# Optimization experiments

Hardware: AMD Instinct MI355X
Metric: run time of the kernel (lower is better)

The kernel has to match this reference:

```python
import jax, jax.numpy as jnp
import numpy as np

N_NODES = 50000
IN_CH = 256
Z_DIM = 64
N_EDGES = 800000


def setup_inputs() -> dict:
    key = jax.random.key(0)
    k_x, k_e, k_wm, k_ws = jax.random.split(key, 4)
    x = jax.random.normal(k_x, (N_NODES, IN_CH), dtype=jnp.float32)
    edge_index = jax.random.randint(k_e, (2, N_EDGES), 0, N_NODES, dtype=jnp.int64)
    # Glorot-style init like PyG GCNConv
    scale = 1.0 / np.sqrt(IN_CH)
    W_mu = jax.random.uniform(k_wm, (IN_CH, Z_DIM), dtype=jnp.float32, minval=-scale, maxval=scale)
    W_logstd = jax.random.uniform(k_ws, (IN_CH, Z_DIM), dtype=jnp.float32, minval=-scale, maxval=scale)
    b_mu = jnp.zeros((Z_DIM,), dtype=jnp.float32)
    b_logstd = jnp.zeros((Z_DIM,), dtype=jnp.float32)
    return {"x": x, "edge_index": edge_index, "W_mu": W_mu, "b_mu": b_mu,
            "W_logstd": W_logstd, "b_logstd": b_logstd}


def _gcn_conv(x, W, b, src, dst, deg_inv_sqrt, num_nodes):
    # PyG GCNConv: out = D^{-1/2} (A + I) D^{-1/2} X W + b
    xw = x @ W                                   # [N, Z]
    norm = deg_inv_sqrt[src] * deg_inv_sqrt[dst]  # [E+N]
    msg = xw[src] * norm[:, None]                 # gather + scale, [E+N, Z]
    agg = jax.ops.segment_sum(msg, dst, num_segments=num_nodes)  # scatter-add
    return agg + b


def reference(x, edge_index, W_mu, b_mu, W_logstd, b_logstd):
    num_nodes = x.shape[0]
    loops = jnp.arange(num_nodes, dtype=edge_index.dtype)
    src = jnp.concatenate([edge_index[0], loops])
    dst = jnp.concatenate([edge_index[1], loops])
    # degree (with self loops) on target nodes, symmetric normalization
    deg = jax.ops.segment_sum(jnp.ones_like(dst, dtype=x.dtype), dst, num_segments=num_nodes)
    deg_inv_sqrt = jnp.where(deg > 0, jax.lax.rsqrt(jnp.maximum(deg, 1.0)), 0.0)
    mu = _gcn_conv(x, W_mu, b_mu, src, dst, deg_inv_sqrt, num_nodes)
    logstd = _gcn_conv(x, W_logstd, b_logstd, src, dst, deg_inv_sqrt, num_nodes)
    return (mu, logstd)
```

## Files before the change

kernel.cpp:

```cpp
#include <hip/hip_runtime.h>

#define N_NODES 50000
#define IN_CH   256
#define Z_DIM   64
#define N_EDGES 800000
#define CH2     128
#define NODE_OFF (N_NODES * Z_DIM)
#define SEG     8
#define SEGN    50048
#define NBUCKET (SEG * SEGN)
#define CAP     16
#define CAPN    64
#define ECHUNKS (N_EDGES / 256)
#define TM      128
#define GTILES  ((N_NODES + TM - 1) / TM)
#define DBLK    ((N_NODES + 31) / 32)
#define NW      32768

typedef __bf16 bf16x8 __attribute__((ext_vector_type(8)));
typedef float  f32x4  __attribute__((ext_vector_type(4)));

__device__ __forceinline__ unsigned short f2bf(float f) {
    __bf16 h = (__bf16)f;
    unsigned short u;
    __builtin_memcpy(&u, &h, 2);
    return u;
}
__device__ __forceinline__ float bf_lo(unsigned w) { return __uint_as_float(w << 16); }
__device__ __forceinline__ float bf_hi(unsigned w) { return __uint_as_float(w & 0xFFFF0000u); }

__global__ void k_pre(int* __restrict__ cur8,
                      const float* __restrict__ Wmu, const float* __restrict__ Wls,
                      unsigned short* __restrict__ WbT) {
    int g = blockIdx.x * 256 + threadIdx.x;
    if (g < NBUCKET) cur8[g] = 0;
    int h = g - NBUCKET;
    if (h >= 0 && h < NW) {
        int n = h >> 8, k = h & 255;
        float v = (n < 64) ? Wmu[(size_t)k * 64 + n] : Wls[(size_t)k * 64 + (n - 64)];
        WbT[(size_t)n * 256 + k] = f2bf(v);
    }
}

#define CSP2 136
__device__ __forceinline__ void gemm_tile(int t, const float* __restrict__ x,
                                          const unsigned short* __restrict__ WbT,
                                          unsigned short* __restrict__ xwb,
                                          unsigned short* As) {
    const int tid = threadIdx.x;
    const int r0  = t * TM;

    {
        int row_l0 = tid >> 3;
        int cb     = (tid & 7) * 32;
#pragma unroll
        for (int r = 0; r < 4; ++r) {
            int row_l = r * 32 + row_l0;
            int row   = r0 + row_l;
            char* dpb = (char*)As + row_l * 512;
            unsigned cswz = (unsigned)((row_l & 7) << 4);
            if (row < N_NODES) {
                const float4* xp = (const float4*)(x + (size_t)row * IN_CH + cb);
#pragma unroll
                for (int i = 0; i < 4; ++i) {
                    float4 a = xp[2 * i];
                    float4 b = xp[2 * i + 1];
                    uint4 w;
                    w.x = (unsigned)f2bf(a.x) | ((unsigned)f2bf(a.y) << 16);
                    w.y = (unsigned)f2bf(a.z) | ((unsigned)f2bf(a.w) << 16);
                    w.z = (unsigned)f2bf(b.x) | ((unsigned)f2bf(b.y) << 16);
                    w.w = (unsigned)f2bf(b.z) | ((unsigned)f2bf(b.w) << 16);
                    *(uint4*)(dpb + (((unsigned)(cb * 2 + i * 16)) ^ cswz)) = w;
                }
            } else {
                uint4 z = make_uint4(0, 0, 0, 0);
#pragma unroll
                for (int i = 0; i < 4; ++i)
                    *(uint4*)(dpb + (((unsigned)(cb * 2 + i * 16)) ^ cswz)) = z;
            }
        }
    }
    __syncthreads();

    const int wv    = tid >> 6;
    const int lane  = tid & 63;
    const int m     = lane & 15;
    const int q     = lane >> 4;
    const int rbase = wv * 32;

    f32x4 acc[2][8] = {};
    const char* apb0 = (const char*)As + (rbase + m) * 512;
    const char* apb1 = apb0 + 16 * 512;
    const unsigned   sw  = (unsigned)((m & 7) << 4);
    const unsigned short* bp = WbT + (size_t)m * 256 + q * 8;

#pragma unroll
    for (int k0 = 0; k0 < IN_CH; k0 += 32) {
        unsigned off = ((unsigned)(q * 16 + 2 * k0)) ^ sw;
        bf16x8 a0 = *(const bf16x8*)(apb0 + off);
        bf16x8 a1 = *(const bf16x8*)(apb1 + off);
#pragma unroll
        for (int nt = 0; nt < 8; ++nt) {
            bf16x8 bf_ = *(const bf16x8*)(bp + (size_t)nt * 16 * 256 + k0);
            acc[0][nt] = __builtin_amdgcn_mfma_f32_16x16x32_bf16(a0, bf_, acc[0][nt], 0, 0, 0);
            acc[1][nt] = __builtin_amdgcn_mfma_f32_16x16x32_bf16(a1, bf_, acc[1][nt], 0, 0, 0);
        }
    }

    __syncthreads();
    {
        unsigned short* Css = As;
#pragma unroll
        for (int mi = 0; mi < 2; ++mi)
#pragma unroll
            for (int nt = 0; nt < 8; ++nt)
#pragma unroll
                for (int r = 0; r < 4; ++r)
                    Css[(rbase + mi * 16 + q * 4 + r) * CSP2 + nt * 16 + m] =
                        f2bf(acc[mi][nt][r]);
    }
    __syncthreads();
    {
        int row_l = tid >> 2;
        int c0    = (tid & 3) * 32;
#pragma unroll
        for (int rr = 0; rr < 2; ++rr) {
            int rl  = rr * 64 + row_l;
            int row = r0 + rl;
            if (row < N_NODES) {
                const uint4* cp = (const uint4*)(As + rl * CSP2 + c0);
                uint4 w0 = cp[0];
                uint4 w1 = cp[1];
                uint4 w2 = cp[2];
                uint4 w3 = cp[3];
                uint4* op = (uint4*)(xwb + (size_t)row * CH2 + c0);
                op[0] = w0; op[1] = w1; op[2] = w2; op[3] = w3;
            }
        }
    }
}

__global__ __launch_bounds__(256, 2) void k_gemm_scat(
    const float* __restrict__ x, const unsigned short* __restrict__ WbT,
    unsigned short* __restrict__ xwb,
    const int* __restrict__ src, const int* __restrict__ dst,
    int* __restrict__ cur8, unsigned short* __restrict__ pk2) {
    __shared__ __align__(16) unsigned short As[TM * 256];
    if (blockIdx.x < GTILES) {
        gemm_tile(blockIdx.x, x, WbT, xwb, As);
    } else {
        int c = blockIdx.x - GTILES;
        int e = c * 256 + threadIdx.x;
        int s = src[e];
        int d = dst[e];
        int idx = (c & (SEG - 1)) * SEGN + d;
        int pos = atomicAdd(&cur8[idx], 1);
        if (pos < CAP) pk2[(size_t)idx * CAP + pos] = (unsigned short)s;
    }
}

__global__ __launch_bounds__(256) void k_dinv(const int* __restrict__ cur8,
                                              const unsigned short* __restrict__ pk2,
                                              float* __restrict__ dinv,
                                              unsigned short* __restrict__ plist,
                                              unsigned short* __restrict__ degc) {
    const int i = blockIdx.x * 32 + (threadIdx.x >> 3);
    const int s = threadIdx.x & 7;
    if (i >= N_NODES) return;

    int cnt = cur8[s * SEGN + i];
    int cc  = (cnt > CAP) ? CAP : cnt;

    int run = cc;
#pragma unroll
    for (int k = 1; k < 8; k <<= 1) {
        int v = __shfl_up(run, k, 8);
        if (s >= k) run += v;
    }
    int tot = cnt;
#pragma unroll
    for (int k = 1; k < 8; k <<= 1) tot += __shfl_xor(tot, k, 8);

    int total_c = __shfl(run, 7, 8);

    int off = run - cc;
    int lim = CAPN - off;
    if (lim < 0) lim = 0;
    if (cc > lim) cc = lim;

    const unsigned short* sp = pk2 + ((size_t)(s * SEGN + i)) * CAP;
    unsigned short*       dp = plist + (size_t)i * CAPN + off;
    for (int j = 0; j < cc; ++j) dp[j] = sp[j];

    if (s == 0) {
        dinv[i] = rsqrtf((float)(1 + tot));
        degc[i] = (unsigned short)((total_c > CAPN) ? CAPN : total_c);
    }
}

__global__ __launch_bounds__(256) void k_gather(const unsigned short* __restrict__ plist,
                                                const unsigned short* __restrict__ degc,
                                                const unsigned short* __restrict__ xwb,
                                                const float* __restrict__ dinv,
                                                const float* __restrict__ bmu,
                                                const float* __restrict__ bls,
                                                float* __restrict__ out) {
    const int i  = blockIdx.x * 16 + (threadIdx.x >> 4);
    const int cl = threadIdx.x & 15;

    const float di  = dinv[i];
    const int   deg = degc[i];

    float acc[8];
    {
        float sq = di * di;
        uint4 w = *(const uint4*)(xwb + (size_t)i * CH2 + cl * 8);
        acc[0] = bf_lo(w.x) * sq; acc[1] = bf_hi(w.x) * sq;
        acc[2] = bf_lo(w.y) * sq; acc[3] = bf_hi(w.y) * sq;
        acc[4] = bf_lo(w.z) * sq; acc[5] = bf_hi(w.z) * sq;
        acc[6] = bf_lo(w.w) * sq; acc[7] = bf_hi(w.w) * sq;
    }

    const unsigned short* lp = plist + (size_t)i * CAPN;
    for (int j = 0; j < deg; j += 4) {
        uint2 pe = *(const uint2*)(lp + j);
        int s0 = (int)(pe.x & 0xFFFFu);
        int s1 = (int)(pe.x >> 16);
        int s2 = (int)(pe.y & 0xFFFFu);
        int s3 = (int)(pe.y >> 16);
        int rem = deg - j;
        int e1 = (rem > 1) ? s1 : s0;
        int e2 = (rem > 2) ? s2 : s0;
        int e3 = (rem > 3) ? s3 : s0;
        float n0 = di * dinv[s0];
        float n1 = (rem > 1) ? di * dinv[e1] : 0.f;
        float n2 = (rem > 2) ? di * dinv[e2] : 0.f;
        float n3 = (rem > 3) ? di * dinv[e3] : 0.f;
        const uint4 w0 = *(const uint4*)(xwb + (size_t)s0 * CH2 + cl * 8);
        const uint4 w1 = *(const uint4*)(xwb + (size_t)e1 * CH2 + cl * 8);
        const uint4 w2 = *(const uint4*)(xwb + (size_t)e2 * CH2 + cl * 8);
        const uint4 w3 = *(const uint4*)(xwb + (size_t)e3 * CH2 + cl * 8);
        acc[0] += bf_lo(w0.x) * n0 + bf_lo(w1.x) * n1 + bf_lo(w2.x) * n2 + bf_lo(w3.x) * n3;
        acc[1] += bf_hi(w0.x) * n0 + bf_hi(w1.x) * n1 + bf_hi(w2.x) * n2 + bf_hi(w3.x) * n3;
        acc[2] += bf_lo(w0.y) * n0 + bf_lo(w1.y) * n1 + bf_lo(w2.y) * n2 + bf_lo(w3.y) * n3;
        acc[3] += bf_hi(w0.y) * n0 + bf_hi(w1.y) * n1 + bf_hi(w2.y) * n2 + bf_hi(w3.y) * n3;
        acc[4] += bf_lo(w0.z) * n0 + bf_lo(w1.z) * n1 + bf_lo(w2.z) * n2 + bf_lo(w3.z) * n3;
        acc[5] += bf_hi(w0.z) * n0 + bf_hi(w1.z) * n1 + bf_hi(w2.z) * n2 + bf_hi(w3.z) * n3;
        acc[6] += bf_lo(w0.w) * n0 + bf_lo(w1.w) * n1 + bf_lo(w2.w) * n2 + bf_lo(w3.w) * n3;
        acc[7] += bf_hi(w0.w) * n0 + bf_hi(w1.w) * n1 + bf_hi(w2.w) * n2 + bf_hi(w3.w) * n3;
    }

    {
        int c0 = cl * 8;
        const float* bb = (c0 < 64) ? (bmu + c0) : (bls + (c0 - 64));
        float4 b0 = *(const float4*)(bb + 0);
        float4 b1 = *(const float4*)(bb + 4);
        float* o = (c0 < 64) ? (out + (size_t)i * 64 + c0)
                             : (out + NODE_OFF + (size_t)i * 64 + (c0 - 64));
        *(float4*)(o + 0) = make_float4(acc[0] + b0.x, acc[1] + b0.y,
                                        acc[2] + b0.z, acc[3] + b0.w);
        *(float4*)(o + 4) = make_float4(acc[4] + b1.x, acc[5] + b1.y,
                                        acc[6] + b1.z, acc[7] + b1.w);
    }
}

extern "C" void kernel_launch(void* const* d_in, const int* in_sizes, int n_in,
                              void* d_out, int out_size, void* d_ws, size_t ws_size,
                              hipStream_t stream) {
    const float* x   = (const float*)d_in[0];
    const int*   ei  = (const int*)d_in[1];
    const float* Wmu = (const float*)d_in[2];
    const float* bmu = (const float*)d_in[3];
    const float* Wls = (const float*)d_in[4];
    const float* bls = (const float*)d_in[5];
    float* out = (float*)d_out;

    const int* src = ei;
    const int* dst = ei + N_EDGES;

    char* ws = (char*)d_ws;
    int*            cur8  = (int*)(ws + 0);
    float*          dinv  = (float*)(ws + 1638400);
    unsigned short* WbT   = (unsigned short*)(ws + 1867776);
    unsigned short* pk2   = (unsigned short*)(ws + 2097152);
    unsigned short* xwb   = (unsigned short*)(ws + 16777216);
    unsigned short* plist = (unsigned short*)(ws + 29577216);
    unsigned short* degc  = (unsigned short*)(ws + 35977216);

    k_pre<<<(NBUCKET + NW + 255) / 256, 256, 0, stream>>>(cur8, Wmu, Wls, WbT);
    k_gemm_scat<<<GTILES + ECHUNKS, 256, 0, stream>>>(x, WbT, xwb, src, dst, cur8, pk2);
    k_dinv<<<DBLK, 256, 0, stream>>>(cur8, pk2, dinv, plist, degc);
    k_gather<<<N_NODES / 16, 256, 0, stream>>>(plist, degc, xwb, dinv, bmu, bls, out);
}
```

Baseline: 183.5 us.

## Fuse degree/list build and gather into one persistent kernel with grid barrier

Merges the k_dinv and k_gather kernels into a single persistent kernel with a fixed grid of 1792 blocks that grid-strides over nodes, joined by a software grid-wide barrier built on agent-scope atomics. The barrier counters are reset in k_pre. This removes one kernel launch and the drain and refill between the two phases, in exchange for spin-wait overhead, reliance on all 1792 blocks being co-resident (a bounded spin is the only guard against deadlock), and lower parallelism from the fixed grid.

```diff
diff --git a/kernel.cpp b/kernel.cpp
--- a/kernel.cpp
+++ b/kernel.cpp
@@ -14,8 +14,8 @@
 #define ECHUNKS (N_EDGES / 256)
 #define TM      128
 #define GTILES  ((N_NODES + TM - 1) / TM)
-#define DBLK    ((N_NODES + 31) / 32)
 #define NW      32768
+#define GRID_B  1792
 
 typedef __bf16 bf16x8 __attribute__((ext_vector_type(8)));
 typedef float  f32x4  __attribute__((ext_vector_type(4)));
@@ -31,9 +31,10 @@
 
 __global__ void k_pre(int* __restrict__ cur8,
                       const float* __restrict__ Wmu, const float* __restrict__ Wls,
-                      unsigned short* __restrict__ WbT) {
+                      unsigned short* __restrict__ WbT, int* __restrict__ bar) {
     int g = blockIdx.x * 256 + threadIdx.x;
     if (g < NBUCKET) cur8[g] = 0;
+    if (g < 2) bar[g] = 0;
     int h = g - NBUCKET;
     if (h >= 0 && h < NW) {
         int n = h >> 8, k = h & 255;
@@ -159,108 +160,129 @@
     }
 }
 
-__global__ __launch_bounds__(256) void k_dinv(const int* __restrict__ cur8,
-                                              const unsigned short* __restrict__ pk2,
-                                              float* __restrict__ dinv,
-                                              unsigned short* __restrict__ plist,
-                                              unsigned short* __restrict__ degc) {
-    const int i = blockIdx.x * 32 + (threadIdx.x >> 3);
-    const int s = threadIdx.x & 7;
-    if (i >= N_NODES) return;
-
-    int cnt = cur8[s * SEGN + i];
-    int cc  = (cnt > CAP) ? CAP : cnt;
-
-    int run = cc;
-#pragma unroll
-    for (int k = 1; k < 8; k <<= 1) {
-        int v = __shfl_up(run, k, 8);
-        if (s >= k) run += v;
-    }
-    int tot = cnt;
-#pragma unroll
-    for (int k = 1; k < 8; k <<= 1) tot += __shfl_xor(tot, k, 8);
-
-    int total_c = __shfl(run, 7, 8);
-
-    int off = run - cc;
-    int lim = CAPN - off;
-    if (lim < 0) lim = 0;
-    if (cc > lim) cc = lim;
-
-    const unsigned short* sp = pk2 + ((size_t)(s * SEGN + i)) * CAP;
-    unsigned short*       dp = plist + (size_t)i * CAPN + off;
-    for (int j = 0; j < cc; ++j) dp[j] = sp[j];
-
-    if (s == 0) {
-        dinv[i] = rsqrtf((float)(1 + tot));
-        degc[i] = (unsigned short)((total_c > CAPN) ? CAPN : total_c);
-    }
-}
-
-__global__ __launch_bounds__(256) void k_gather(const unsigned short* __restrict__ plist,
-                                                const unsigned short* __restrict__ degc,
-                                                const unsigned short* __restrict__ xwb,
-                                                const float* __restrict__ dinv,
-                                                const float* __restrict__ bmu,
-                                                const float* __restrict__ bls,
-                                                float* __restrict__ out) {
-    const int i  = blockIdx.x * 16 + (threadIdx.x >> 4);
-    const int cl = threadIdx.x & 15;
-
-    const float di  = dinv[i];
-    const int   deg = degc[i];
-
-    float acc[8];
-    {
-        float sq = di * di;
-        uint4 w = *(const uint4*)(xwb + (size_t)i * CH2 + cl * 8);
-        acc[0] = bf_lo(w.x) * sq; acc[1] = bf_hi(w.x) * sq;
-        acc[2] = bf_lo(w.y) * sq; acc[3] = bf_hi(w.y) * sq;
-        acc[4] = bf_lo(w.z) * sq; acc[5] = bf_hi(w.z) * sq;
-        acc[6] = bf_lo(w.w) * sq; acc[7] = bf_hi(w.w) * sq;
-    }
-
-    const unsigned short* lp = plist + (size_t)i * CAPN;
-    for (int j = 0; j < deg; j += 4) {
-        uint2 pe = *(const uint2*)(lp + j);
-        int s0 = (int)(pe.x & 0xFFFFu);
-        int s1 = (int)(pe.x >> 16);
-        int s2 = (int)(pe.y & 0xFFFFu);
-        int s3 = (int)(pe.y >> 16);
-        int rem = deg - j;
-        int e1 = (rem > 1) ? s1 : s0;
-        int e2 = (rem > 2) ? s2 : s0;
-        int e3 = (rem > 3) ? s3 : s0;
-        float n0 = di * dinv[s0];
-        float n1 = (rem > 1) ? di * dinv[e1] : 0.f;
-        float n2 = (rem > 2) ? di * dinv[e2] : 0.f;
-        float n3 = (rem > 3) ? di * dinv[e3] : 0.f;
-        const uint4 w0 = *(const uint4*)(xwb + (size_t)s0 * CH2 + cl * 8);
-        const uint4 w1 = *(const uint4*)(xwb + (size_t)e1 * CH2 + cl * 8);
-        const uint4 w2 = *(const uint4*)(xwb + (size_t)e2 * CH2 + cl * 8);
-        const uint4 w3 = *(const uint4*)(xwb + (size_t)e3 * CH2 + cl * 8);
-        acc[0] += bf_lo(w0.x) * n0 + bf_lo(w1.x) * n1 + bf_lo(w2.x) * n2 + bf_lo(w3.x) * n3;
-        acc[1] += bf_hi(w0.x) * n0 + bf_hi(w1.x) * n1 + bf_hi(w2.x) * n2 + bf_hi(w3.x) * n3;
-        acc[2] += bf_lo(w0.y) * n0 + bf_lo(w1.y) * n1 + bf_lo(w2.y) * n2 + bf_lo(w3.y) * n3;
-        acc[3] += bf_hi(w0.y) * n0 + bf_hi(w1.y) * n1 + bf_hi(w2.y) * n2 + bf_hi(w3.y) * n3;
-        acc[4] += bf_lo(w0.z) * n0 + bf_lo(w1.z) * n1 + bf_lo(w2.z) * n2 + bf_lo(w3.z) * n3;
-        acc[5] += bf_hi(w0.z) * n0 + bf_hi(w1.z) * n1 + bf_hi(w2.z) * n2 + bf_hi(w3.z) * n3;
-        acc[6] += bf_lo(w0.w) * n0 + bf_lo(w1.w) * n1 + bf_lo(w2.w) * n2 + bf_lo(w3.w) * n3;
-        acc[7] += bf_hi(w0.w) * n0 + bf_hi(w1.w) * n1 + bf_hi(w2.w) * n2 + bf_hi(w3.w) * n3;
-    }
-
-    {
-        int c0 = cl * 8;
-        const float* bb = (c0 < 64) ? (bmu + c0) : (bls + (c0 - 64));
-        float4 b0 = *(const float4*)(bb + 0);
-        float4 b1 = *(const float4*)(bb + 4);
-        float* o = (c0 < 64) ? (out + (size_t)i * 64 + c0)
-                             : (out + NODE_OFF + (size_t)i * 64 + (c0 - 64));
-        *(float4*)(o + 0) = make_float4(acc[0] + b0.x, acc[1] + b0.y,
-                                        acc[2] + b0.z, acc[3] + b0.w);
-        *(float4*)(o + 4) = make_float4(acc[4] + b1.x, acc[5] + b1.y,
-                                        acc[6] + b1.z, acc[7] + b1.w);
+__device__ __forceinline__ void sw_barrier(int* __restrict__ bar, int nblk) {
+    __syncthreads();
+    if (threadIdx.x == 0) {
+        __threadfence();
+        int prev = __hip_atomic_fetch_add(&bar[0], 1, __ATOMIC_ACQ_REL,
+                                          __HIP_MEMORY_SCOPE_AGENT);
+        if (prev == nblk - 1) {
+            __hip_atomic_store(&bar[1], 1, __ATOMIC_RELEASE, __HIP_MEMORY_SCOPE_AGENT);
+        } else {
+            int spins = 0;
+            while (__hip_atomic_load(&bar[1], __ATOMIC_ACQUIRE,
+                                     __HIP_MEMORY_SCOPE_AGENT) == 0) {
+                __builtin_amdgcn_s_sleep(8);
+                if (++spins > (1 << 24)) break;
+            }
+        }
+    }
+    __syncthreads();
+}
+
+__global__ __launch_bounds__(256, 8) void k_fuse_b(
+    const int* __restrict__ cur8, const unsigned short* __restrict__ pk2,
+    float* __restrict__ dinv, unsigned short* __restrict__ plist,
+    unsigned short* __restrict__ degc, const unsigned short* __restrict__ xwb,
+    const float* __restrict__ bmu, const float* __restrict__ bls,
+    float* __restrict__ out, int* __restrict__ bar) {
+
+    {
+        const int s = threadIdx.x & 7;
+        const int stride = (int)(gridDim.x * 32);
+        for (int i = blockIdx.x * 32 + (threadIdx.x >> 3); i < N_NODES; i += stride) {
+            int cnt = cur8[s * SEGN + i];
+            int cc  = (cnt > CAP) ? CAP : cnt;
+
+            int run = cc;
+#pragma unroll
+            for (int k = 1; k < 8; k <<= 1) {
+                int v = __shfl_up(run, k, 8);
+                if (s >= k) run += v;
+            }
+            int tot = cnt;
+#pragma unroll
+            for (int k = 1; k < 8; k <<= 1) tot += __shfl_xor(tot, k, 8);
+
+            int total_c = __shfl(run, 7, 8);
+
+            int off = run - cc;
+            int lim = CAPN - off;
+            if (lim < 0) lim = 0;
+            if (cc > lim) cc = lim;
+
+            const unsigned short* sp = pk2 + ((size_t)(s * SEGN + i)) * CAP;
+            unsigned short*       dp = plist + (size_t)i * CAPN + off;
+            for (int j = 0; j < cc; ++j) dp[j] = sp[j];
+
+            if (s == 0) {
+                dinv[i] = rsqrtf((float)(1 + tot));
+                degc[i] = (unsigned short)((total_c > CAPN) ? CAPN : total_c);
+            }
+        }
+    }
+
+    sw_barrier(bar, (int)gridDim.x);
+
+    {
+        const int cl = threadIdx.x & 15;
+        const int stride = (int)(gridDim.x * 16);
+        for (int i = blockIdx.x * 16 + (threadIdx.x >> 4); i < N_NODES; i += stride) {
+            const float di  = dinv[i];
+            const int   deg = degc[i];
+
+            float acc[8];
+            {
+                float sq = di * di;
+                uint4 w = *(const uint4*)(xwb + (size_t)i * CH2 + cl * 8);
+                acc[0] = bf_lo(w.x) * sq; acc[1] = bf_hi(w.x) * sq;
+                acc[2] = bf_lo(w.y) * sq; acc[3] = bf_hi(w.y) * sq;
+                acc[4] = bf_lo(w.z) * sq; acc[5] = bf_hi(w.z) * sq;
+                acc[6] = bf_lo(w.w) * sq; acc[7] = bf_hi(w.w) * sq;
+            }
+
+            const unsigned short* lp = plist + (size_t)i * CAPN;
+            for (int j = 0; j < deg; j += 4) {
+                uint2 pe = *(const uint2*)(lp + j);
+                int s0 = (int)(pe.x & 0xFFFFu);
+                int s1 = (int)(pe.x >> 16);
+                int s2 = (int)(pe.y & 0xFFFFu);
+                int s3 = (int)(pe.y >> 16);
+                int rem = deg - j;
+                int e1 = (rem > 1) ? s1 : s0;
+                int e2 = (rem > 2) ? s2 : s0;
+                int e3 = (rem > 3) ? s3 : s0;
+                float n0 = di * dinv[s0];
+                float n1 = (rem > 1) ? di * dinv[e1] : 0.f;
+                float n2 = (rem > 2) ? di * dinv[e2] : 0.f;
+                float n3 = (rem > 3) ? di * dinv[e3] : 0.f;
+                const uint4 w0 = *(const uint4*)(xwb + (size_t)s0 * CH2 + cl * 8);
+                const uint4 w1 = *(const uint4*)(xwb + (size_t)e1 * CH2 + cl * 8);
+                const uint4 w2 = *(const uint4*)(xwb + (size_t)e2 * CH2 + cl * 8);
+                const uint4 w3 = *(const uint4*)(xwb + (size_t)e3 * CH2 + cl * 8);
+                acc[0] += bf_lo(w0.x) * n0 + bf_lo(w1.x) * n1 + bf_lo(w2.x) * n2 + bf_lo(w3.x) * n3;
+                acc[1] += bf_hi(w0.x) * n0 + bf_hi(w1.x) * n1 + bf_hi(w2.x) * n2 + bf_hi(w3.x) * n3;
+                acc[2] += bf_lo(w0.y) * n0 + bf_lo(w1.y) * n1 + bf_lo(w2.y) * n2 + bf_lo(w3.y) * n3;
+                acc[3] += bf_hi(w0.y) * n0 + bf_hi(w1.y) * n1 + bf_hi(w2.y) * n2 + bf_hi(w3.y) * n3;
+                acc[4] += bf_lo(w0.z) * n0 + bf_lo(w1.z) * n1 + bf_lo(w2.z) * n2 + bf_lo(w3.z) * n3;
+                acc[5] += bf_hi(w0.z) * n0 + bf_hi(w1.z) * n1 + bf_hi(w2.z) * n2 + bf_hi(w3.z) * n3;
+                acc[6] += bf_lo(w0.w) * n0 + bf_lo(w1.w) * n1 + bf_lo(w2.w) * n2 + bf_lo(w3.w) * n3;
+                acc[7] += bf_hi(w0.w) * n0 + bf_hi(w1.w) * n1 + bf_hi(w2.w) * n2 + bf_hi(w3.w) * n3;
+            }
+
+            {
+                int c0 = cl * 8;
+                const float* bb = (c0 < 64) ? (bmu + c0) : (bls + (c0 - 64));
+                float4 b0 = *(const float4*)(bb + 0);
+                float4 b1 = *(const float4*)(bb + 4);
+                float* o = (c0 < 64) ? (out + (size_t)i * 64 + c0)
+                                     : (out + NODE_OFF + (size_t)i * 64 + (c0 - 64));
+                *(float4*)(o + 0) = make_float4(acc[0] + b0.x, acc[1] + b0.y,
+                                                acc[2] + b0.z, acc[3] + b0.w);
+                *(float4*)(o + 4) = make_float4(acc[4] + b1.x, acc[5] + b1.y,
+                                                acc[6] + b1.z, acc[7] + b1.w);
+            }
+        }
     }
 }
 
@@ -280,6 +302,7 @@
 
     char* ws = (char*)d_ws;
     int*            cur8  = (int*)(ws + 0);
+    int*            bar   = (int*)(ws + 1601536);
     float*          dinv  = (float*)(ws + 1638400);
     unsigned short* WbT   = (unsigned short*)(ws + 1867776);
     unsigned short* pk2   = (unsigned short*)(ws + 2097152);
@@ -287,8 +310,8 @@
     unsigned short* plist = (unsigned short*)(ws + 29577216);
     unsigned short* degc  = (unsigned short*)(ws + 35977216);
 
-    k_pre<<<(NBUCKET + NW + 255) / 256, 256, 0, stream>>>(cur8, Wmu, Wls, WbT);
+    k_pre<<<(NBUCKET + NW + 255) / 256, 256, 0, stream>>>(cur8, Wmu, Wls, WbT, bar);
     k_gemm_scat<<<GTILES + ECHUNKS, 256, 0, stream>>>(x, WbT, xwb, src, dst, cur8, pk2);
-    k_dinv<<<DBLK, 256, 0, stream>>>(cur8, pk2, dinv, plist, degc);
-    k_gather<<<N_NODES / 16, 256, 0, stream>>>(plist, degc, xwb, dinv, bmu, bls, out);
-}
+    k_fuse_b<<<GRID_B, 256, 0, stream>>>(cur8, pk2, dinv, plist, degc, xwb,
+                                         bmu, bls, out, bar);
+}
```

New measurement: 395.9 us. 2.16x slower.
